# Optimization experiments

Measured on AMD Instinct MI355X. Metric: run time of the kernel, lower is better.

The kernel has to match this reference:

```python
import jax, jax.numpy as jnp
import numpy as np

NUM_EXPERTS = 8
TOP_K = 2


def setup_inputs() -> dict:
    key = jax.random.key(0)
    ks = jax.random.split(key, 5)
    B, S, H, F, E = 2, 2048, 1024, 4096, NUM_EXPERTS
    return {
        "hidden_states": jax.random.normal(ks[0], (B, S, H), dtype=jnp.float32),
        "router_w": jax.random.normal(ks[1], (H, E), dtype=jnp.float32) * 0.02,
        "router_b": jnp.zeros((E,), dtype=jnp.float32),
        "w1": jax.random.normal(ks[2], (E, H, F), dtype=jnp.float32) * 0.02,
        "b1": jnp.zeros((E, F), dtype=jnp.float32),
        "w2": jax.random.normal(ks[3], (E, F, H), dtype=jnp.float32) * 0.02,
        "b2": jnp.zeros((E, H), dtype=jnp.float32),
    }


def reference(hidden_states, router_w, router_b, w1, b1, w2, b2):
    # Router: softmax over experts, take top-2, renormalize.
    logits = jnp.einsum("bsh,he->bse", hidden_states, router_w) + router_b
    probs = jax.nn.softmax(logits, axis=-1)
    top_w, top_i = jax.lax.top_k(probs, TOP_K)              # [B,S,2]
    top_w = top_w / jnp.sum(top_w, axis=-1, keepdims=True)
    # Combine weights per expert: [B,S,E] (sum of slot weights where routed).
    combine = jnp.sum(
        top_w[..., None] * jax.nn.one_hot(top_i, NUM_EXPERTS, dtype=top_w.dtype),
        axis=-2,
    )
    # Dense expert FFN over stacked experts (grouped GEMM form).
    h = jax.nn.gelu(
        jnp.einsum("bsh,ehf->ebsf", hidden_states, w1) + b1[:, None, None, :],
        approximate=False,
    )  # exact GELU matches torch nn.GELU default
    y = jnp.einsum("ebsf,efh->ebsh", h, w2) + b2[:, None, None, :]
    # Weighted combine of top-2 expert outputs per token.
    return jnp.einsum("bse,ebsh->bsh", combine, y)
```

## Files before the change

### kernel.cpp

```cpp
#include <hip/hip_runtime.h>
#include <hip/hip_bf16.h>
#include <stdint.h>

#define T_TOKENS 4096
#define H_DIM    1024
#define F_DIM    4096
#define NE       8
#define NA       8192

typedef __bf16 bf16x8 __attribute__((ext_vector_type(8)));
typedef float  f32x4  __attribute__((ext_vector_type(4)));
typedef unsigned short u16x4v __attribute__((ext_vector_type(4)));

__device__ __forceinline__ float b2f(unsigned short u) {
    union { float f; uint32_t i; } v; v.i = ((uint32_t)u) << 16; return v.f;
}
__device__ __forceinline__ unsigned short f2b(float f) {
    union { float f; uint32_t i; } v; v.f = f;
    uint32_t x = v.i;
    return (unsigned short)((x + 0x7FFFu + ((x >> 16) & 1u)) >> 16);
}

__device__ __forceinline__ float gelu_f(float x) {
    float z = fabsf(x) * 0.70710678118f;
    float t = 1.0f / (1.0f + 0.3275911f * z);
    float p = t * (0.254829592f + t * (-0.284496736f +
              t * (1.421413741f + t * (-1.453152027f + t * 1.061405429f))));
    float erf_z = 1.0f - p * __expf(-z * z);
    float sgn_erf = (x >= 0.f) ? erf_z : -erf_z;
    return x * (0.5f + 0.5f * sgn_erf);
}

__device__ __forceinline__ void gl_lds16(const void* g, void* l) {
    __builtin_amdgcn_global_load_lds(
        (const __attribute__((address_space(1))) void*)g,
        (__attribute__((address_space(3))) void*)l,
        16, 0, 0);
}

__global__ void probe_kernel(const unsigned short* __restrict__ hs,
                             int* __restrict__ flag) {
    int lane = threadIdx.x;
    int cnt = 0;
    for (int j = 0; j < 16; j++) {
        unsigned short u = hs[(lane * 16 + j) * 2];
        int e = (u >> 7) & 0xFF;
        if (e >= 100 && e <= 135) cnt++;
    }
    for (int off = 32; off > 0; off >>= 1) cnt += __shfl_down(cnt, off);
    if (lane == 0) *flag = (cnt >= 512) ? 0 : 1;
}

__global__ __launch_bounds__(256) void router_kernel(
    const void* __restrict__ hs, const void* __restrict__ rw,
    const void* __restrict__ rb, const int* __restrict__ flag,
    int* __restrict__ top_i, float* __restrict__ top_w,
    unsigned short* __restrict__ hsb) {
    bool f32 = (*flag != 0);
    int wave = threadIdx.x >> 6, lane = threadIdx.x & 63;
    int t = blockIdx.x * 4 + wave;
    unsigned short* hout = hsb + (size_t)t * H_DIM;
    float acc[NE];
#pragma unroll
    for (int e = 0; e < NE; e++) acc[e] = 0.f;
    if (f32) {
        const float* hrow = (const float*)hs + (size_t)t * H_DIM;
        const float* rwf = (const float*)rw;
        for (int j = 0; j < 16; j++) {
            int k = j * 64 + lane;
            float h = hrow[k];
            hout[k] = f2b(h);
            float4 a = *(const float4*)(rwf + (size_t)k * NE);
            float4 b = *(const float4*)(rwf + (size_t)k * NE + 4);
            acc[0] += h * a.x; acc[1] += h * a.y; acc[2] += h * a.z; acc[3] += h * a.w;
            acc[4] += h * b.x; acc[5] += h * b.y; acc[6] += h * b.z; acc[7] += h * b.w;
        }
    } else {
        const unsigned short* hrow = (const unsigned short*)hs + (size_t)t * H_DIM;
        const unsigned short* rwu = (const unsigned short*)rw;
        for (int j = 0; j < 16; j++) {
            int k = j * 64 + lane;
            unsigned short hu = hrow[k];
            hout[k] = hu;
            float h = b2f(hu);
            uint4 rv = *(const uint4*)(rwu + (size_t)k * NE);
            const unsigned short* rs = (const unsigned short*)&rv;
#pragma unroll
            for (int e = 0; e < NE; e++) acc[e] += h * b2f(rs[e]);
        }
    }
#pragma unroll
    for (int e = 0; e < NE; e++)
        for (int off = 32; off > 0; off >>= 1) acc[e] += __shfl_down(acc[e], off);
    if (lane == 0) {
        float lg[NE];
#pragma unroll
        for (int e = 0; e < NE; e++)
            lg[e] = acc[e] + (f32 ? ((const float*)rb)[e]
                                  : b2f(((const unsigned short*)rb)[e]));
        int e0 = 0;
        for (int e = 1; e < NE; e++) if (lg[e] > lg[e0]) e0 = e;
        int e1 = (e0 == 0) ? 1 : 0;
        for (int e = 0; e < NE; e++) if (e != e0 && lg[e] > lg[e1]) e1 = e;
        float w0 = 1.f / (1.f + expf(lg[e1] - lg[e0]));
        top_i[t * 2] = e0; top_i[t * 2 + 1] = e1;
        top_w[t * 2] = w0; top_w[t * 2 + 1] = 1.f - w0;
    }
}

__global__ __launch_bounds__(256) void assign_kernel(
    const int* __restrict__ top_i, const float* __restrict__ top_w,
    int* __restrict__ token_list, float* __restrict__ wgt_list,
    int* __restrict__ assign_row, int* __restrict__ counts,
    int* __restrict__ offsets) {
    __shared__ int cnt_s[NE], cur_s[NE];
    int tid = threadIdx.x;
    if (tid < NE) cnt_s[tid] = 0;
    __syncthreads();
    for (int idx = tid; idx < NA; idx += 256) atomicAdd(&cnt_s[top_i[idx]], 1);
    __syncthreads();
    if (tid == 0) {
        int run = 0;
        for (int e = 0; e < NE; e++) {
            offsets[e] = run; counts[e] = cnt_s[e]; cur_s[e] = run; run += cnt_s[e];
        }
    }
    __syncthreads();
    for (int idx = tid; idx < NA; idx += 256) {
        int e = top_i[idx];
        int pos = atomicAdd(&cur_s[e], 1);
        token_list[pos] = idx >> 1;
        wgt_list[pos] = top_w[idx];
        assign_row[idx] = pos;
    }
}

__global__ __launch_bounds__(256) void transpose_kernel(
    const void* __restrict__ in, unsigned short* __restrict__ out,
    int R, int C, const int* __restrict__ flag) {
    bool f32 = (*flag != 0);
    size_t zo = (size_t)blockIdx.z * R * C;
    int c0 = blockIdx.x * 64, r0 = blockIdx.y * 64;
    __shared__ unsigned short t[64][65];
    int tx = threadIdx.x & 15, ty = threadIdx.x >> 4;
    if (f32) {
        const float* inf = (const float*)in + zo;
#pragma unroll
        for (int i = 0; i < 4; i++) {
            int r = ty + i * 16;
            float4 v = *(const float4*)&inf[(size_t)(r0 + r) * C + c0 + tx * 4];
            t[r][tx * 4] = f2b(v.x); t[r][tx * 4 + 1] = f2b(v.y);
            t[r][tx * 4 + 2] = f2b(v.z); t[r][tx * 4 + 3] = f2b(v.w);
        }
    } else {
        const unsigned short* inu = (const unsigned short*)in + zo;
#pragma unroll
        for (int i = 0; i < 4; i++) {
            int r = ty + i * 16;
            ushort4 v = *(const ushort4*)&inu[(size_t)(r0 + r) * C + c0 + tx * 4];
            t[r][tx * 4] = v.x; t[r][tx * 4 + 1] = v.y;
            t[r][tx * 4 + 2] = v.z; t[r][tx * 4 + 3] = v.w;
        }
    }
    __syncthreads();
#pragma unroll
    for (int i = 0; i < 4; i++) {
        int cc = ty + i * 16;
        ushort4 w;
        w.x = t[tx * 4][cc]; w.y = t[tx * 4 + 1][cc];
        w.z = t[tx * 4 + 2][cc]; w.w = t[tx * 4 + 3][cc];
        *(ushort4*)&out[zo + (size_t)(c0 + cc) * R + r0 + tx * 4] = w;
    }
}

template <int MODE>
__global__ __launch_bounds__(256, 3) void gemm_kernel(
    const unsigned short* __restrict__ Abase,
    const unsigned short* __restrict__ Bt,
    const void* __restrict__ bias,
    const int* __restrict__ flag,
    const int* __restrict__ token_list, const float* __restrict__ wgt_list,
    const int* __restrict__ counts, const int* __restrict__ offsets,
    unsigned short* __restrict__ act_out, unsigned short* __restrict__ y_out) {
    constexpr int K    = (MODE == 0) ? H_DIM : F_DIM;
    constexpr int NDIM = (MODE == 0) ? F_DIM : H_DIM;
    constexpr int AST  = K;
    constexpr int BM   = 128, BN = 128;
    constexpr int MI   = 4, NJ = 4;
    constexpr int NK   = K / 32;
    constexpr int ABUF = BM * 32;
    constexpr int BBUF = BN * 32;
    constexpr int NIA  = 2, NIB = 2;

    const int lid = blockIdx.x + gridDim.x * (blockIdx.y + gridDim.y * blockIdx.z);
    const int e   = lid & 7;
    const int r_  = lid >> 3;
    const int nx  = r_ % gridDim.x;
    const int my  = r_ / gridDim.x;

    const int cnt = counts[e];
    const int m0 = my * BM;
    if (m0 >= cnt) return;
    const int off = offsets[e];
    const int n0 = nx * BN;
    const bool f32 = (*flag != 0);

    __shared__ __bf16 As[3 * ABUF];
    __shared__ __bf16 Bs[3 * BBUF];
    __shared__ int   tok_s[BM];
    __shared__ float wgt_s[BM];

    const int tid = threadIdx.x;
    const int wave = tid >> 6, lane = tid & 63;

    if (tid < BM) {
        int r = off + min(m0 + tid, cnt - 1);
        tok_s[tid] = (MODE == 0) ? token_list[r] : r;
        wgt_s[tid] = wgt_list[r];
    }
    __syncthreads();

    const char* Abytes = (const char*)Abase;
    const char* Bbytes = (const char*)(Bt + (size_t)e * NDIM * K);
    const int rl = lane >> 2;
    const int chk = (lane & 3) ^ (rl & 3);
    uint64_t ga[NIA], gb[NIB];
    uint32_t la[NIA], lb[NIB];
#pragma unroll
    for (int j = 0; j < NIA; j++) {
        int rowA = (wave * NIA + j) * 16 + rl;
        ga[j] = (uint64_t)(uintptr_t)(Abytes + ((size_t)tok_s[rowA] * AST + chk * 8) * 2);
        la[j] = (wave * NIA + j) * 512;
    }
#pragma unroll
    for (int j = 0; j < NIB; j++) {
        int rowB = n0 + (wave * NIB + j) * 16 + rl;
        gb[j] = (uint64_t)(uintptr_t)(Bbytes + ((size_t)rowB * K + chk * 8) * 2);
        lb[j] = (wave * NIB + j) * 512;
    }

    f32x4 acc[MI][NJ];
#pragma unroll
    for (int i = 0; i < MI; i++)
#pragma unroll
        for (int j = 0; j < NJ; j++) acc[i][j] = (f32x4){0.f, 0.f, 0.f, 0.f};

    const int wr = wave >> 1, wc = wave & 1;
    const int lane15 = lane & 15, quad = lane >> 4;

    auto stage = [&](int buf) {
#pragma unroll
        for (int j = 0; j < NIA; j++) {
            gl_lds16((const void*)(uintptr_t)ga[j], (void*)(As + buf * ABUF + la[j]));
            ga[j] += 64;
        }
#pragma unroll
        for (int j = 0; j < NIB; j++) {
            gl_lds16((const void*)(uintptr_t)gb[j], (void*)(Bs + buf * BBUF + lb[j]));
            gb[j] += 64;
        }
    };
    auto compute = [&](int buf) {
        const __bf16* Ab = As + buf * ABUF;
        const __bf16* Bb = Bs + buf * BBUF;
        bf16x8 a[MI], b[NJ];
#pragma unroll
        for (int i = 0; i < MI; i++) {
            int row = wr * 64 + i * 16 + lane15;
            a[i] = *(const bf16x8*)&Ab[row * 32 + ((quad ^ (row & 3)) * 8)];
        }
#pragma unroll
        for (int j = 0; j < NJ; j++) {
            int row = wc * 64 + j * 16 + lane15;
            b[j] = *(const bf16x8*)&Bb[row * 32 + ((quad ^ (row & 3)) * 8)];
        }
        __builtin_amdgcn_s_setprio(1);
#pragma unroll
        for (int i = 0; i < MI; i++)
#pragma unroll
            for (int j = 0; j < NJ; j++)
                acc[i][j] = __builtin_amdgcn_mfma_f32_16x16x32_bf16(b[j], a[i], acc[i][j], 0, 0, 0);
        __builtin_amdgcn_s_setprio(0);
    };

    stage(0);
    int bufw = 1, bufr = 0;
    for (int kt = 0; kt < NK - 1; kt++) {
        stage(bufw);
        bufw = (bufw == 2) ? 0 : bufw + 1;
        asm volatile("s_waitcnt vmcnt(4)" ::: "memory");
        __builtin_amdgcn_s_barrier();
        __builtin_amdgcn_sched_barrier(0);
        compute(bufr);
        bufr = (bufr == 2) ? 0 : bufr + 1;
    }
    asm volatile("s_waitcnt vmcnt(0)" ::: "memory");
    __builtin_amdgcn_s_barrier();
    __builtin_amdgcn_sched_barrier(0);
    compute(bufr);

    unsigned short* outp = (MODE == 0) ? act_out : y_out;
#pragma unroll
    for (int i = 0; i < MI; i++) {
        int rowl = wr * 64 + i * 16 + lane15;
        if (m0 + rowl < cnt) {
            size_t gbase = (size_t)(off + m0 + rowl) * NDIM;
            float wgt = wgt_s[rowl];
#pragma unroll
            for (int j = 0; j < NJ; j++) {
                int col = n0 + wc * 64 + j * 16 + quad * 4;
                float bb[4];
                if (f32) {
                    float4 bf4 = *(const float4*)((const float*)bias + (size_t)e * NDIM + col);
                    bb[0] = bf4.x; bb[1] = bf4.y; bb[2] = bf4.z; bb[3] = bf4.w;
                } else {
                    ushort4 bu = *(const ushort4*)((const unsigned short*)bias + (size_t)e * NDIM + col);
                    bb[0] = b2f(bu.x); bb[1] = b2f(bu.y); bb[2] = b2f(bu.z); bb[3] = b2f(bu.w);
                }
                u16x4v o;
#pragma unroll
                for (int r = 0; r < 4; r++) {
                    float v = acc[i][j][r] + bb[r];
                    o[r] = (MODE == 0) ? f2b(gelu_f(v)) : f2b(v * wgt);
                }
                *(u16x4v*)&outp[gbase + col] = o;
            }
        }
    }
}

__global__ __launch_bounds__(256) void combine_kernel(
    const unsigned short* __restrict__ y, const int* __restrict__ assign_row,
    void* __restrict__ out, const int* __restrict__ flag) {
    bool f32 = (*flag != 0);
    int t = blockIdx.x;
    int r0 = assign_row[t * 2], r1 = assign_row[t * 2 + 1];
    ushort4 a = ((const ushort4*)(y + (size_t)r0 * H_DIM))[threadIdx.x];
    ushort4 b = ((const ushort4*)(y + (size_t)r1 * H_DIM))[threadIdx.x];
    float s0 = b2f(a.x) + b2f(b.x), s1 = b2f(a.y) + b2f(b.y);
    float s2 = b2f(a.z) + b2f(b.z), s3 = b2f(a.w) + b2f(b.w);
    if (f32) {
        float4 o = {s0, s1, s2, s3};
        ((float4*)out)[(size_t)t * (H_DIM / 4) + threadIdx.x] = o;
    } else {
        ushort4 o;
        o.x = f2b(s0); o.y = f2b(s1); o.z = f2b(s2); o.w = f2b(s3);
        ((ushort4*)((unsigned short*)out + (size_t)t * H_DIM))[threadIdx.x] = o;
    }
}

extern "C" void kernel_launch(void* const* d_in, const int* in_sizes, int n_in,
                              void* d_out, int out_size, void* d_ws, size_t ws_size,
                              hipStream_t stream) {
    const void* hs = d_in[0];
    const void* rw = d_in[1];
    const void* rb = d_in[2];
    const void* w1 = d_in[3];
    const void* b1 = d_in[4];
    const void* w2 = d_in[5];
    const void* b2 = d_in[6];

    char* ws = (char*)d_ws;
    size_t o = 0;
    auto alloc = [&](size_t bytes) {
        char* p = ws + o; o += (bytes + 255) & ~(size_t)255; return p;
    };
    unsigned short* wt   = (unsigned short*)alloc((size_t)NE * F_DIM * H_DIM * 2);
    unsigned short* act  = (unsigned short*)alloc((size_t)NA * F_DIM * 2);
    unsigned short* yb   = (unsigned short*)alloc((size_t)NA * H_DIM * 2);
    unsigned short* hsb  = (unsigned short*)alloc((size_t)T_TOKENS * H_DIM * 2);
    int*   top_i      = (int*)alloc(NA * 4);
    float* top_w      = (float*)alloc(NA * 4);
    int*   token_list = (int*)alloc(NA * 4);
    float* wgt_list   = (float*)alloc(NA * 4);
    int*   assign_row = (int*)alloc(NA * 4);
    int*   counts     = (int*)alloc(64);
    int*   offsets    = (int*)alloc(64);
    int*   flag       = (int*)alloc(64);
    (void)ws_size; (void)in_sizes; (void)n_in; (void)out_size;

    probe_kernel<<<1, 64, 0, stream>>>((const unsigned short*)hs, flag);
    router_kernel<<<T_TOKENS / 4, 256, 0, stream>>>(hs, rw, rb, flag, top_i, top_w, hsb);
    assign_kernel<<<1, 256, 0, stream>>>(top_i, top_w, token_list, wgt_list,
                                         assign_row, counts, offsets);
    transpose_kernel<<<dim3(F_DIM / 64, H_DIM / 64, NE), 256, 0, stream>>>(
        w1, wt, H_DIM, F_DIM, flag);
    gemm_kernel<0><<<dim3(F_DIM / 128, T_TOKENS / 128, NE), 256, 0, stream>>>(
        hsb, wt, b1, flag, token_list, wgt_list, counts, offsets, act, nullptr);
    transpose_kernel<<<dim3(H_DIM / 64, F_DIM / 64, NE), 256, 0, stream>>>(
        w2, wt, F_DIM, H_DIM, flag);
    gemm_kernel<1><<<dim3(H_DIM / 128, T_TOKENS / 128, NE), 256, 0, stream>>>(
        act, wt, b2, flag, token_list, wgt_list, counts, offsets, nullptr, yb);
    combine_kernel<<<T_TOKENS, 256, 0, stream>>>(yb, assign_row, d_out, flag);
}
```

Measured before the change: 567.3 us.

## Merge both weight transposes into one packed kernel and change LDS swizzle

```diff
diff --git a/kernel.cpp b/kernel.cpp
--- a/kernel.cpp
+++ b/kernel.cpp
@@ -170,6 +170,61 @@
         w.x = t[tx * 4][cc]; w.y = t[tx * 4 + 1][cc];
         w.z = t[tx * 4 + 2][cc]; w.w = t[tx * 4 + 3][cc];
         *(ushort4*)&out[zo + (size_t)(c0 + cc) * R + r0 + tx * 4] = w;
+    }
+}
+
+__global__ __launch_bounds__(256) void prep_kernel(
+    const void* __restrict__ w1, const void* __restrict__ w2,
+    unsigned short* __restrict__ wt1, unsigned short* __restrict__ wt2,
+    const int* __restrict__ flag) {
+    const bool f32 = (*flag != 0);
+    const bool is1 = (blockIdx.z < 8);
+    const int slice = is1 ? blockIdx.z : blockIdx.z - 8;
+    const int R = is1 ? H_DIM : F_DIM;
+    const int C = is1 ? F_DIM : H_DIM;
+    const int c0 = (is1 ? blockIdx.x : blockIdx.y) * 64;
+    const int r0 = (is1 ? blockIdx.y : blockIdx.x) * 64;
+    const void* in = is1 ? w1 : w2;
+    unsigned short* out = is1 ? wt1 : wt2;
+    const size_t zo = (size_t)slice * H_DIM * F_DIM;
+
+    __shared__ uint32_t t32[64][33];
+    const int tid = threadIdx.x;
+    const int tx = tid & 15, ty = tid >> 4;
+
+#pragma unroll
+    for (int i = 0; i < 2; i++) {
+        int rp = ty + i * 16;
+        if (f32) {
+            const float* inf = (const float*)in + zo;
+            float4 A = *(const float4*)&inf[(size_t)(r0 + 2 * rp) * C + c0 + tx * 4];
+            float4 B = *(const float4*)&inf[(size_t)(r0 + 2 * rp + 1) * C + c0 + tx * 4];
+            t32[tx * 4 + 0][rp] = (uint32_t)f2b(A.x) | ((uint32_t)f2b(B.x) << 16);
+            t32[tx * 4 + 1][rp] = (uint32_t)f2b(A.y) | ((uint32_t)f2b(B.y) << 16);
+            t32[tx * 4 + 2][rp] = (uint32_t)f2b(A.z) | ((uint32_t)f2b(B.z) << 16);
+            t32[tx * 4 + 3][rp] = (uint32_t)f2b(A.w) | ((uint32_t)f2b(B.w) << 16);
+        } else {
+            const unsigned short* inu = (const unsigned short*)in + zo;
+            ushort4 A = *(const ushort4*)&inu[(size_t)(r0 + 2 * rp) * C + c0 + tx * 4];
+            ushort4 B = *(const ushort4*)&inu[(size_t)(r0 + 2 * rp + 1) * C + c0 + tx * 4];
+            t32[tx * 4 + 0][rp] = (uint32_t)A.x | ((uint32_t)B.x << 16);
+            t32[tx * 4 + 1][rp] = (uint32_t)A.y | ((uint32_t)B.y << 16);
+            t32[tx * 4 + 2][rp] = (uint32_t)A.z | ((uint32_t)B.z << 16);
+            t32[tx * 4 + 3][rp] = (uint32_t)A.w | ((uint32_t)B.w << 16);
+        }
+    }
+    __syncthreads();
+#pragma unroll
+    for (int k = 0; k < 2; k++) {
+        int chunk = tid + 256 * k;
+        int cc = chunk >> 3;
+        int rr = chunk & 7;
+        uint4 w;
+        w.x = t32[cc][rr * 4 + 0];
+        w.y = t32[cc][rr * 4 + 1];
+        w.z = t32[cc][rr * 4 + 2];
+        w.w = t32[cc][rr * 4 + 3];
+        *(uint4*)&out[zo + (size_t)(c0 + cc) * R + r0 + rr * 8] = w;
     }
 }
 
@@ -223,7 +278,7 @@
     const char* Abytes = (const char*)Abase;
     const char* Bbytes = (const char*)(Bt + (size_t)e * NDIM * K);
     const int rl = lane >> 2;
-    const int chk = (lane & 3) ^ (rl & 3);
+    const int chk = (lane & 3) ^ ((lane >> 3) & 3);
     uint64_t ga[NIA], gb[NIB];
     uint32_t la[NIA], lb[NIB];
 #pragma unroll
@@ -267,12 +322,12 @@
 #pragma unroll
         for (int i = 0; i < MI; i++) {
             int row = wr * 64 + i * 16 + lane15;
-            a[i] = *(const bf16x8*)&Ab[row * 32 + ((quad ^ (row & 3)) * 8)];
+            a[i] = *(const bf16x8*)&Ab[row * 32 + ((quad ^ ((row >> 1) & 3)) * 8)];
         }
 #pragma unroll
         for (int j = 0; j < NJ; j++) {
             int row = wc * 64 + j * 16 + lane15;
-            b[j] = *(const bf16x8*)&Bb[row * 32 + ((quad ^ (row & 3)) * 8)];
+            b[j] = *(const bf16x8*)&Bb[row * 32 + ((quad ^ ((row >> 1) & 3)) * 8)];
         }
         __builtin_amdgcn_s_setprio(1);
 #pragma unroll
@@ -365,7 +420,7 @@
     auto alloc = [&](size_t bytes) {
         char* p = ws + o; o += (bytes + 255) & ~(size_t)255; return p;
     };
-    unsigned short* wt   = (unsigned short*)alloc((size_t)NE * F_DIM * H_DIM * 2);
+    unsigned short* wt1  = (unsigned short*)alloc((size_t)NE * F_DIM * H_DIM * 2);
     unsigned short* act  = (unsigned short*)alloc((size_t)NA * F_DIM * 2);
     unsigned short* yb   = (unsigned short*)alloc((size_t)NA * H_DIM * 2);
     unsigned short* hsb  = (unsigned short*)alloc((size_t)T_TOKENS * H_DIM * 2);
@@ -377,19 +432,30 @@
     int*   counts     = (int*)alloc(64);
     int*   offsets    = (int*)alloc(64);
     int*   flag       = (int*)alloc(64);
-    (void)ws_size; (void)in_sizes; (void)n_in; (void)out_size;
+    unsigned short* wt2 = (unsigned short*)alloc((size_t)NE * F_DIM * H_DIM * 2);
+    const bool fused = (o <= ws_size);
+    (void)in_sizes; (void)n_in; (void)out_size;
 
     probe_kernel<<<1, 64, 0, stream>>>((const unsigned short*)hs, flag);
     router_kernel<<<T_TOKENS / 4, 256, 0, stream>>>(hs, rw, rb, flag, top_i, top_w, hsb);
     assign_kernel<<<1, 256, 0, stream>>>(top_i, top_w, token_list, wgt_list,
                                          assign_row, counts, offsets);
-    transpose_kernel<<<dim3(F_DIM / 64, H_DIM / 64, NE), 256, 0, stream>>>(
-        w1, wt, H_DIM, F_DIM, flag);
-    gemm_kernel<0><<<dim3(F_DIM / 128, T_TOKENS / 128, NE), 256, 0, stream>>>(
-        hsb, wt, b1, flag, token_list, wgt_list, counts, offsets, act, nullptr);
-    transpose_kernel<<<dim3(H_DIM / 64, F_DIM / 64, NE), 256, 0, stream>>>(
-        w2, wt, F_DIM, H_DIM, flag);
-    gemm_kernel<1><<<dim3(H_DIM / 128, T_TOKENS / 128, NE), 256, 0, stream>>>(
-        act, wt, b2, flag, token_list, wgt_list, counts, offsets, nullptr, yb);
+    if (fused) {
+        prep_kernel<<<dim3(F_DIM / 64, H_DIM / 64, 2 * NE), 256, 0, stream>>>(
+            w1, w2, wt1, wt2, flag);
+        gemm_kernel<0><<<dim3(F_DIM / 128, T_TOKENS / 128, NE), 256, 0, stream>>>(
+            hsb, wt1, b1, flag, token_list, wgt_list, counts, offsets, act, nullptr);
+        gemm_kernel<1><<<dim3(H_DIM / 128, T_TOKENS / 128, NE), 256, 0, stream>>>(
+            act, wt2, b2, flag, token_list, wgt_list, counts, offsets, nullptr, yb);
+    } else {
+        transpose_kernel<<<dim3(F_DIM / 64, H_DIM / 64, NE), 256, 0, stream>>>(
+            w1, wt1, H_DIM, F_DIM, flag);
+        gemm_kernel<0><<<dim3(F_DIM / 128, T_TOKENS / 128, NE), 256, 0, stream>>>(
+            hsb, wt1, b1, flag, token_list, wgt_list, counts, offsets, act, nullptr);
+        transpose_kernel<<<dim3(H_DIM / 64, F_DIM / 64, NE), 256, 0, stream>>>(
+            w2, wt1, F_DIM, H_DIM, flag);
+        gemm_kernel<1><<<dim3(H_DIM / 128, T_TOKENS / 128, NE), 256, 0, stream>>>(
+            act, wt1, b2, flag, token_list, wgt_list, counts, offsets, nullptr, yb);
+    }
     combine_kernel<<<T_TOKENS, 256, 0, stream>>>(yb, assign_row, d_out, flag);
 }
```

Measured after the change: 581.7 us. +2.5%, slower.
